# Optimization experiments

Hardware: AMD Instinct MI355X
Metric: run time of the kernel (lower is better)

## Reference

```python
import jax, jax.numpy as jnp
import numpy as np

B, T, NTYPES, D = 1_000_000, 5, 2, 6

def setup_inputs() -> dict:
    key = jax.random.key(0)
    k1, k2 = jax.random.split(key)
    visible_treats = jax.random.uniform(k1, (B, T, NTYPES, D), dtype=jnp.float32)
    vision = jax.random.randint(k2, (B, T), 0, 2, dtype=jnp.int32)
    return {"visible_treats": visible_treats, "vision": vision}

def reference(visible_treats, vision):
    # visible_treats: [B, T, 2, 6]; vision: [B, T] (0/1)
    Tn = visible_treats.shape[1]
    seen = vision.astype(bool)[:, :, None]                      # [B, T, 1]
    has_treat = jnp.max(visible_treats[..., :5], axis=-1) > 0.5  # [B, T, 2]
    valid = seen & has_treat                                     # [B, T, 2]
    # last valid timestep per (batch, treat_type); -1 if none
    t_ids = jnp.arange(Tn, dtype=jnp.int32)[None, :, None]
    last_t = jnp.max(jnp.where(valid, t_ids, -1), axis=1)        # [B, 2]
    found = last_t >= 0                                          # [B, 2]
    safe_t = jnp.maximum(last_t, 0)                              # [B, 2]
    # gather visible_treats[b, last_t[b,tt], tt, :]
    gathered = jnp.take_along_axis(
        visible_treats, safe_t[:, None, :, None], axis=1
    )[:, 0]                                                      # [B, 2, 6]
    default = jnp.zeros((visible_treats.shape[-1],), visible_treats.dtype).at[5].set(1.0)
    return jnp.where(found[:, :, None], gathered, default)       # [B, 2, 6]
```

## Files before the change

kernel.cpp:

```cpp
#include <hip/hip_runtime.h>


__global__ __launch_bounds__(256) void belief_kernel(
    const float4* __restrict__ vt4,
    const int*    __restrict__ vision,
    float4*       __restrict__ out4,
    int B)
{
    int b = blockIdx.x * blockDim.x + threadIdx.x;
    if (b >= B) return;

    const float4* p = vt4 + (size_t)b * 15;
    float f[60];
#pragma unroll
    for (int k = 0; k < 15; ++k) {
        float4 r = p[k];
        f[4*k + 0] = r.x;
        f[4*k + 1] = r.y;
        f[4*k + 2] = r.z;
        f[4*k + 3] = r.w;
    }

    const int* vp = vision + (size_t)b * 5;
    int v[5];
#pragma unroll
    for (int t = 0; t < 5; ++t) v[t] = vp[t];

    float o[12];
#pragma unroll
    for (int tt = 0; tt < 2; ++tt) {
        o[tt*6 + 0] = 0.f; o[tt*6 + 1] = 0.f; o[tt*6 + 2] = 0.f;
        o[tt*6 + 3] = 0.f; o[tt*6 + 4] = 0.f; o[tt*6 + 5] = 1.f;
    }

#pragma unroll
    for (int t = 0; t < 5; ++t) {
#pragma unroll
        for (int tt = 0; tt < 2; ++tt) {
            const int base = t*12 + tt*6;
            float m = f[base + 0];
            m = fmaxf(m, f[base + 1]);
            m = fmaxf(m, f[base + 2]);
            m = fmaxf(m, f[base + 3]);
            m = fmaxf(m, f[base + 4]);
            bool valid = (v[t] != 0) && (m > 0.5f);
            if (valid) {
#pragma unroll
                for (int d = 0; d < 6; ++d) o[tt*6 + d] = f[base + d];
            }
        }
    }

    float4* op = out4 + (size_t)b * 3;
    op[0] = make_float4(o[0], o[1], o[2],  o[3]);
    op[1] = make_float4(o[4], o[5], o[6],  o[7]);
    op[2] = make_float4(o[8], o[9], o[10], o[11]);
}

extern "C" void kernel_launch(void* const* d_in, const int* in_sizes, int n_in,
                              void* d_out, int out_size, void* d_ws, size_t ws_size,
                              hipStream_t stream) {
    const float4* vt4   = (const float4*)d_in[0];
    const int*    vision = (const int*)d_in[1];
    float4*       out4  = (float4*)d_out;
    int B = in_sizes[1] / 5;

    int block = 256;
    int grid  = (B + block - 1) / block;
    belief_kernel<<<grid, block, 0, stream>>>(vt4, vision, out4, B);
}
```

Measured before the change: 61.70 us.

## Stage input through LDS with direct global-to-LDS loads and coalesced output stores

Replaces per-thread strided float4 loads (stride 15 float4s per thread) with wave-coalesced global_load_lds transfers into a 60KB shared buffer, then each thread reads its row from LDS. Output is also staged through LDS so global stores are contiguous across threads. The aim is fully coalesced DRAM traffic for a bandwidth-bound kernel. In exchange, the large LDS footprint limits occupancy to about two blocks per CU and adds barriers.

```diff
diff --git a/kernel.cpp b/kernel.cpp
--- a/kernel.cpp
+++ b/kernel.cpp
@@ -1,5 +1,13 @@
 #include <hip/hip_runtime.h>
 
+
+#define WPB 256
+
+__device__ __forceinline__ void gload_lds16(const void* g, void* l) {
+    __builtin_amdgcn_global_load_lds(
+        (const __attribute__((address_space(1))) void*)g,
+        (__attribute__((address_space(3))) void*)l, 16, 0, 0);
+}
 
 __global__ __launch_bounds__(256) void belief_kernel(
     const float4* __restrict__ vt4,
@@ -7,65 +15,91 @@
     float4*       __restrict__ out4,
     int B)
 {
-    int b = blockIdx.x * blockDim.x + threadIdx.x;
-    if (b >= B) return;
+    __shared__ float4 s_vt[WPB * 15];
 
-    const float4* p = vt4 + (size_t)b * 15;
-    float f[60];
+    const int tid  = threadIdx.x;
+    const int lane = tid & 63;
+    const int wave = tid >> 6;
+
+    const int blockBase = blockIdx.x * WPB;
+    const int f4Total   = B * 15;
+    const int f4Base    = blockBase * 15;
+
 #pragma unroll
-    for (int k = 0; k < 15; ++k) {
-        float4 r = p[k];
-        f[4*k + 0] = r.x;
-        f[4*k + 1] = r.y;
-        f[4*k + 2] = r.z;
-        f[4*k + 3] = r.w;
+    for (int i = 0; i < 15; ++i) {
+        const int l = i * 256 + wave * 64;
+        int g = f4Base + l + lane;
+        if (g >= f4Total) g = f4Total - 1;
+        gload_lds16(vt4 + g, &s_vt[l]);
     }
 
-    const int* vp = vision + (size_t)b * 5;
-    int v[5];
+    const int b = blockBase + tid;
+    int v[5] = {0, 0, 0, 0, 0};
+    if (b < B) {
+        const int* vp = vision + b * 5;
 #pragma unroll
-    for (int t = 0; t < 5; ++t) v[t] = vp[t];
+        for (int t = 0; t < 5; ++t) v[t] = vp[t];
+    }
+
+    __syncthreads();
 
     float o[12];
 #pragma unroll
     for (int tt = 0; tt < 2; ++tt) {
-        o[tt*6 + 0] = 0.f; o[tt*6 + 1] = 0.f; o[tt*6 + 2] = 0.f;
-        o[tt*6 + 3] = 0.f; o[tt*6 + 4] = 0.f; o[tt*6 + 5] = 1.f;
+        o[tt*6+0]=0.f; o[tt*6+1]=0.f; o[tt*6+2]=0.f;
+        o[tt*6+3]=0.f; o[tt*6+4]=0.f; o[tt*6+5]=1.f;
     }
 
+    const int fbase = tid * 15;
 #pragma unroll
     for (int t = 0; t < 5; ++t) {
-#pragma unroll
-        for (int tt = 0; tt < 2; ++tt) {
-            const int base = t*12 + tt*6;
-            float m = f[base + 0];
-            m = fmaxf(m, f[base + 1]);
-            m = fmaxf(m, f[base + 2]);
-            m = fmaxf(m, f[base + 3]);
-            m = fmaxf(m, f[base + 4]);
+        float4 r0 = s_vt[fbase + t*3 + 0];
+        float4 r1 = s_vt[fbase + t*3 + 1];
+        float4 r2 = s_vt[fbase + t*3 + 2];
+
+        {
+            float m = fmaxf(fmaxf(fmaxf(r0.x, r0.y), fmaxf(r0.z, r0.w)), r1.x);
             bool valid = (v[t] != 0) && (m > 0.5f);
             if (valid) {
-#pragma unroll
-                for (int d = 0; d < 6; ++d) o[tt*6 + d] = f[base + d];
+                o[0]=r0.x; o[1]=r0.y; o[2]=r0.z; o[3]=r0.w; o[4]=r1.x; o[5]=r1.y;
+            }
+        }
+        {
+            float m = fmaxf(fmaxf(fmaxf(r1.z, r1.w), fmaxf(r2.x, r2.y)), r2.z);
+            bool valid = (v[t] != 0) && (m > 0.5f);
+            if (valid) {
+                o[6]=r1.z; o[7]=r1.w; o[8]=r2.x; o[9]=r2.y; o[10]=r2.z; o[11]=r2.w;
             }
         }
     }
 
-    float4* op = out4 + (size_t)b * 3;
-    op[0] = make_float4(o[0], o[1], o[2],  o[3]);
-    op[1] = make_float4(o[4], o[5], o[6],  o[7]);
-    op[2] = make_float4(o[8], o[9], o[10], o[11]);
+    __syncthreads();
+
+    float4* s_out = s_vt;
+    s_out[tid*3 + 0] = make_float4(o[0], o[1], o[2],  o[3]);
+    s_out[tid*3 + 1] = make_float4(o[4], o[5], o[6],  o[7]);
+    s_out[tid*3 + 2] = make_float4(o[8], o[9], o[10], o[11]);
+
+    __syncthreads();
+
+    const int oTotal = B * 3;
+    const int oBase  = blockBase * 3;
+#pragma unroll
+    for (int i = 0; i < 3; ++i) {
+        const int l = i * 256 + tid;
+        const int g = oBase + l;
+        if (g < oTotal) out4[g] = s_out[l];
+    }
 }
 
 extern "C" void kernel_launch(void* const* d_in, const int* in_sizes, int n_in,
                               void* d_out, int out_size, void* d_ws, size_t ws_size,
                               hipStream_t stream) {
-    const float4* vt4   = (const float4*)d_in[0];
+    const float4* vt4    = (const float4*)d_in[0];
     const int*    vision = (const int*)d_in[1];
-    float4*       out4  = (float4*)d_out;
+    float4*       out4   = (float4*)d_out;
     int B = in_sizes[1] / 5;
 
-    int block = 256;
-    int grid  = (B + block - 1) / block;
-    belief_kernel<<<grid, block, 0, stream>>>(vt4, vision, out4, B);
+    int grid = (B + WPB - 1) / WPB;
+    belief_kernel<<<grid, WPB, 0, stream>>>(vt4, vision, out4, B);
 }
```

Result: faster. 51.17 us (-17.1%).
